# Optimization experiments

Measured on AMD Instinct MI355X. Metric: run time of the kernel, lower is better.

Reference implementation:

```python
import jax, jax.numpy as jnp
import numpy as np

BN_EPS = 1e-5


def _gin_layer(x, src, dst, W1, b1, W2, b2, gamma, beta):
    N = x.shape[0]
    # scatter-add neighbor aggregation (GINConv with eps=0)
    agg = jax.ops.segment_sum(x[src], dst, num_segments=N)
    h = x + agg
    # MLP: Linear -> ReLU -> Linear
    h = jax.nn.relu(h @ W1 + b1) @ W2 + b2
    # BatchNorm1d (training-mode batch statistics, biased variance)
    mean = jnp.mean(h, axis=0)
    var = jnp.mean(jnp.square(h - mean), axis=0)
    h = (h - mean) * jax.lax.rsqrt(var + BN_EPS) * gamma + beta
    return jax.nn.relu(h)


def setup_inputs() -> dict:
    key = jax.random.key(0)
    ks = jax.random.split(key, 16)
    N, E, F_IN, H, L, G, T = 100000, 400000, 128, 256, 5, 4096, 12
    x = jax.random.normal(ks[0], (N, F_IN), dtype=jnp.float32)
    edge_index = jax.random.randint(ks[1], (2, E), 0, N, dtype=jnp.int64)
    batch_idx = jnp.sort(jax.random.randint(ks[2], (N,), 0, G, dtype=jnp.int64))
    s = 0.02
    inp = {
        "x": x,
        "edge_index": edge_index,
        "batch_idx": batch_idx,
        "num_graphs": G,
        # layer 0: 128 -> 256
        "W1_0": jax.random.normal(ks[3], (F_IN, H), dtype=jnp.float32) * s,
        "b1_0": jnp.zeros((H,), jnp.float32),
        "W2_0": jax.random.normal(ks[4], (H, H), dtype=jnp.float32) * s,
        "b2_0": jnp.zeros((H,), jnp.float32),
        "gamma_0": jnp.ones((H,), jnp.float32),
        "beta_0": jnp.zeros((H,), jnp.float32),
        # layers 1..4 stacked: 256 -> 256
        "W1s": jax.random.normal(ks[5], (L - 1, H, H), dtype=jnp.float32) * s,
        "b1s": jnp.zeros((L - 1, H), jnp.float32),
        "W2s": jax.random.normal(ks[6], (L - 1, H, H), dtype=jnp.float32) * s,
        "b2s": jnp.zeros((L - 1, H), jnp.float32),
        "gammas": jnp.ones((L - 1, H), jnp.float32),
        "betas": jnp.zeros((L - 1, H), jnp.float32),
        # predictor
        "Wp1": jax.random.normal(ks[7], (H, H), dtype=jnp.float32) * s,
        "bp1": jnp.zeros((H,), jnp.float32),
        "Wp2": jax.random.normal(ks[8], (H, T), dtype=jnp.float32) * s,
        "bp2": jnp.zeros((T,), jnp.float32),
    }
    return inp


def reference(x, edge_index, batch_idx, num_graphs,
              W1_0, b1_0, W2_0, b2_0, gamma_0, beta_0,
              W1s, b1s, W2s, b2s, gammas, betas,
              Wp1, bp1, Wp2, bp2):
    src, dst = edge_index[0], edge_index[1]
    h = _gin_layer(x, src, dst, W1_0, b1_0, W2_0, b2_0, gamma_0, beta_0)
    for i in range(W1s.shape[0]):
        h = _gin_layer(h, src, dst, W1s[i], b1s[i], W2s[i], b2s[i], gammas[i], betas[i])
    # global mean pool over graphs
    sums = jax.ops.segment_sum(h, batch_idx, num_segments=num_graphs)
    counts = jax.ops.segment_sum(jnp.ones((h.shape[0],), h.dtype), batch_idx, num_segments=num_graphs)
    g = sums / jnp.maximum(counts, 1.0)[:, None]
    # predictor MLP (dropout=0 in eval)
    out = jax.nn.relu(g @ Wp1 + bp1) @ Wp2 + bp2
    return out
```

## Files before the change

### kernel.cpp

```cpp
#include <hip/hip_runtime.h>


typedef __attribute__((ext_vector_type(4))) float f32x4;
typedef __attribute__((ext_vector_type(8))) _Float16 f16x8;

__device__ __forceinline__ float h2f(unsigned short u) {
  _Float16 h; __builtin_memcpy(&h, &u, 2); return (float)h;
}
__device__ __forceinline__ unsigned short f2h16(float f) {
  _Float16 h = (_Float16)f; unsigned short u; __builtin_memcpy(&u, &h, 2); return u;
}
__device__ __forceinline__ unsigned short f2b(float f) {
  union { float f; unsigned int i; } c; c.f = f;
  unsigned int x = c.i;
  return (unsigned short)((x + 0x7fffu + ((x >> 16) & 1u)) >> 16);
}
__device__ __forceinline__ float lin(const void* p, long long i, int wf32) {
  if (wf32) return ((const float*)p)[i];
  union { unsigned int i; float f; } c;
  c.i = ((unsigned int)((const unsigned short*)p)[i]) << 16;
  return c.f;
}
__device__ __forceinline__ int ldidx(const int* p, long long i, int w64) {
  return w64 ? p[2 * i] : p[i];
}

__global__ void detect_k(const int* __restrict__ edge, const unsigned short* __restrict__ xa,
                         int* __restrict__ flags) {
  if (threadIdx.x != 0 || blockIdx.x != 0) return;
  int nzOdd = 0;
  for (int t = 0; t < 256; t++) if (edge[2 * t + 1] != 0) nzOdd++;
  flags[0] = (nzOdd == 0) ? 1 : 0;
  int plaus = 0;
  for (int t = 0; t < 64; t++) {
    unsigned short w = xa[2 * t];
    int e = (w >> 7) & 0xFF;
    if (w == 0 || (e >= 0x70 && e <= 0x85)) plaus++;
  }
  flags[1] = (plaus < 32) ? 1 : 0;
}

__global__ void zero_i32_k(int* __restrict__ p, int n) {
  int i = blockIdx.x * blockDim.x + threadIdx.x;
  if (i < n) p[i] = 0;
}

__global__ void prep_k(const void* __restrict__ b1, const void* __restrict__ b2,
                       const void* __restrict__ gm, const void* __restrict__ bt, int eoff,
                       float* __restrict__ pb1, float* __restrict__ pb2,
                       float* __restrict__ pg, float* __restrict__ pb,
                       float* __restrict__ gsum, const int* __restrict__ flags) {
  int wf32 = flags[1], t = threadIdx.x;
  pb1[t] = lin(b1, (long long)eoff + t, wf32);
  pb2[t] = lin(b2, (long long)eoff + t, wf32);
  pg[t]  = lin(gm, (long long)eoff + t, wf32);
  pb[t]  = lin(bt, (long long)eoff + t, wf32);
  gsum[t] = 0.f; gsum[256 + t] = 0.f;
}
__global__ void copy256_k(const void* __restrict__ src, int eoff, float* __restrict__ dst,
                          const int* __restrict__ flags) {
  dst[threadIdx.x] = lin(src, (long long)eoff + threadIdx.x, flags[1]);
}

__global__ void transpose_off_k(const void* __restrict__ src, long long eoff,
                                unsigned short* __restrict__ dst, int R, int C,
                                const int* __restrict__ flags) {
  int wf32 = flags[1];
  __shared__ unsigned short t[32][33];
  int bx = blockIdx.x * 32, by = blockIdx.y * 32;
  int x = bx + threadIdx.x;
  for (int i = 0; i < 32; i += 8) {
    int y = by + threadIdx.y + i;
    if (y < R && x < C)
      t[threadIdx.y + i][threadIdx.x] = f2h16(lin(src, eoff + (long long)y * C + x, wf32));
  }
  __syncthreads();
  int x2 = by + threadIdx.x;
  for (int i = 0; i < 32; i += 8) {
    int y = bx + threadIdx.y + i;
    if (y < C && x2 < R) dst[(long long)y * R + x2] = t[threadIdx.x][threadIdx.y + i];
  }
}

__global__ void hist_k(const int* __restrict__ edge, int E, int* __restrict__ cnt,
                       const int* __restrict__ flags) {
  int w64 = flags[0];
  int e = blockIdx.x * blockDim.x + threadIdx.x;
  if (e < E) atomicAdd(&cnt[ldidx(edge, (long long)E + e, w64)], 1);
}
#define SCAN_CHUNK 1024
__global__ void scan1_k(const int* __restrict__ in, int* __restrict__ out,
                        int* __restrict__ partials, int n) {
  __shared__ int sh[256];
  int tid = threadIdx.x;
  int base = blockIdx.x * SCAN_CHUNK + tid * 4;
  int v[4]; int tsum = 0;
#pragma unroll
  for (int i = 0; i < 4; i++) { v[i] = (base + i < n) ? in[base + i] : 0; tsum += v[i]; }
  sh[tid] = tsum; __syncthreads();
  for (int off = 1; off < 256; off <<= 1) {
    int t = (tid >= off) ? sh[tid - off] : 0;
    __syncthreads();
    sh[tid] += t;
    __syncthreads();
  }
  int run = sh[tid] - tsum;
#pragma unroll
  for (int i = 0; i < 4; i++) { if (base + i < n) out[base + i] = run; run += v[i]; }
  if (tid == 255) partials[blockIdx.x] = sh[255];
}
__global__ void scan2_k(int* partials, int B) {
  __shared__ int sh[256];
  int tid = threadIdx.x;
  int orig = (tid < B) ? partials[tid] : 0;
  sh[tid] = orig; __syncthreads();
  for (int off = 1; off < 256; off <<= 1) {
    int t = (tid >= off) ? sh[tid - off] : 0;
    __syncthreads();
    sh[tid] += t;
    __syncthreads();
  }
  if (tid < B) partials[tid] = sh[tid] - orig;
}
__global__ void scan3_k(int* __restrict__ out, const int* __restrict__ partials,
                        int n, int total) {
  int base = blockIdx.x * SCAN_CHUNK + threadIdx.x * 4;
  int add = partials[blockIdx.x];
#pragma unroll
  for (int i = 0; i < 4; i++) { if (base + i < n) out[base + i] += add; }
  if (blockIdx.x == 0 && threadIdx.x == 0) out[n] = total;
}
__global__ void fill_k(const int* __restrict__ edge, int E, const int* __restrict__ rowptr,
                       int* __restrict__ cnt, int* __restrict__ colidx,
                       const int* __restrict__ flags) {
  int w64 = flags[0];
  int e = blockIdx.x * blockDim.x + threadIdx.x;
  if (e >= E) return;
  int s = ldidx(edge, e, w64);
  int d = ldidx(edge, (long long)E + e, w64);
  int p = atomicAdd(&cnt[d], 1);
  colidx[rowptr[d] + p] = s;
}
__global__ void graph_bounds_k(const int* __restrict__ b, int Nn, int G,
                               int* __restrict__ gstart, const int* __restrict__ flags) {
  int w64 = flags[0];
  int g = blockIdx.x * blockDim.x + threadIdx.x;
  if (g > G) return;
  int lo = 0, hi = Nn;
  while (lo < hi) {
    int mid = (lo + hi) >> 1;
    if (ldidx(b, mid, w64) < g) lo = mid + 1; else hi = mid;
  }
  gstart[g] = lo;
}

__global__ void convert_k(const void* __restrict__ x, unsigned short* __restrict__ xh,
                          long long n, const int* __restrict__ flags) {
  int wf32 = flags[1];
  long long base = ((long long)blockIdx.x * blockDim.x + threadIdx.x) * 4;
  if (base >= n) return;
#pragma unroll
  for (int k = 0; k < 4; k++) xh[base + k] = f2h16(lin(x, base + k, wf32));
}

template <int LPN, int APPLY>
__global__ void gather_fused_k(const unsigned short* __restrict__ src,
                               const float* __restrict__ scale, const float* __restrict__ shift,
                               const int* __restrict__ rowptr, const int* __restrict__ colidx,
                               unsigned short* __restrict__ u, int Nn) {
  const int F = LPN * 8;
  int gid = blockIdx.x * blockDim.x + threadIdx.x;
  int node = gid / LPN;
  if (node >= Nn) return;
  int fb = (gid % LPN) * 8;
  float sc[8], sh[8];
  if (APPLY) {
#pragma unroll
    for (int k = 0; k < 8; k++) { sc[k] = scale[fb + k]; sh[k] = shift[fb + k]; }
  }
  float acc[8];
  {
    uint4 raw = *(const uint4*)(src + (long long)node * F + fb);
    unsigned int ws[4] = {raw.x, raw.y, raw.z, raw.w};
#pragma unroll
    for (int k = 0; k < 8; k++) {
      float xv = h2f((unsigned short)((ws[k >> 1] >> ((k & 1) * 16)) & 0xffff));
      acc[k] = APPLY ? fmaxf(xv * sc[k] + sh[k], 0.f) : xv;
    }
  }
  int s = rowptr[node], e = rowptr[node + 1];
  for (int j = s; j < e; j++) {
    long long nb = colidx[j];
    uint4 raw = *(const uint4*)(src + nb * F + fb);
    unsigned int ws[4] = {raw.x, raw.y, raw.z, raw.w};
#pragma unroll
    for (int k = 0; k < 8; k++) {
      float xv = h2f((unsigned short)((ws[k >> 1] >> ((k & 1) * 16)) & 0xffff));
      acc[k] += APPLY ? fmaxf(xv * sc[k] + sh[k], 0.f) : xv;
    }
  }
  uint4 o;
  unsigned int wo[4];
#pragma unroll
  for (int p = 0; p < 4; p++)
    wo[p] = (unsigned int)f2h16(acc[2 * p]) | ((unsigned int)f2h16(acc[2 * p + 1]) << 16);
  o.x = wo[0]; o.y = wo[1]; o.z = wo[2]; o.w = wo[3];
  *(uint4*)(u + (long long)node * F + fb) = o;
}

#define SA 40
#define SP 136
__global__ __launch_bounds__(256) void gemm_k(
    const unsigned short* __restrict__ A, const unsigned short* __restrict__ Bt,
    const float* __restrict__ bias, unsigned short* __restrict__ C,
    int M, int K, int relu, float* __restrict__ gsum) {
  __shared__ __align__(16) unsigned short smem[128 * SP];
  unsigned short* As = smem;
  unsigned short* Bs = smem + 128 * SA;
  int m0 = blockIdx.x * 128, n0 = blockIdx.y * 128;
  int tid = threadIdx.x;
  int wave = tid >> 6, lane = tid & 63;
  int wm = (wave >> 1) * 64, wn = (wave & 1) * 64;
  int lrow = lane & 15, lq = lane >> 4;
  f32x4 acc[4][4] = {};
  int ktiles = K >> 5;
  int srow = tid >> 2;
  int ch8 = (tid & 3) << 3;
  int rowA0 = m0 + srow;      rowA0 = rowA0 < M ? rowA0 : M - 1;
  int rowA1 = m0 + srow + 64; rowA1 = rowA1 < M ? rowA1 : M - 1;
  const unsigned short* pa0 = A + (long long)rowA0 * K + ch8;
  const unsigned short* pa1 = A + (long long)rowA1 * K + ch8;
  const unsigned short* pq0 = Bt + (long long)(n0 + srow) * K + ch8;
  const unsigned short* pq1 = Bt + (long long)(n0 + srow + 64) * K + ch8;
  uint4 va0 = *(const uint4*)pa0, va1 = *(const uint4*)pa1;
  uint4 vb0 = *(const uint4*)pq0, vb1 = *(const uint4*)pq1;
  int lo0 = srow * SA + ch8, lo1 = (srow + 64) * SA + ch8;
  for (int kt = 0; kt < ktiles; ++kt) {
    __syncthreads();
    *(uint4*)(As + lo0) = va0;
    *(uint4*)(As + lo1) = va1;
    *(uint4*)(Bs + lo0) = vb0;
    *(uint4*)(Bs + lo1) = vb1;
    __syncthreads();
    f16x8 af[4], bf[4];
#pragma unroll
    for (int r = 0; r < 4; r++)
      af[r] = *(const f16x8*)(As + (wm + 16 * r + lrow) * SA + lq * 8);
#pragma unroll
    for (int c = 0; c < 4; c++)
      bf[c] = *(const f16x8*)(Bs + (wn + 16 * c + lrow) * SA + lq * 8);
    if (kt + 1 < ktiles) {
      int kb = (kt + 1) << 5;
      va0 = *(const uint4*)(pa0 + kb); va1 = *(const uint4*)(pa1 + kb);
      vb0 = *(const uint4*)(pq0 + kb); vb1 = *(const uint4*)(pq1 + kb);
    }
#pragma unroll
    for (int r = 0; r < 4; r++)
#pragma unroll
      for (int c = 0; c < 4; c++)
        acc[r][c] = __builtin_amdgcn_mfma_f32_16x16x32_f16(af[r], bf[c], acc[r][c], 0, 0, 0);
  }
  __syncthreads();
  unsigned short* Ct = smem;
#pragma unroll
  for (int c = 0; c < 4; c++) {
    int col = wn + 16 * c + lrow;
    float bv = bias[n0 + col];
#pragma unroll
    for (int r = 0; r < 4; r++) {
      int rbase = wm + 16 * r + lq * 4;
#pragma unroll
      for (int i = 0; i < 4; i++) {
        float v = acc[r][c][i] + bv;
        if (relu) v = fmaxf(v, 0.f);
        Ct[(rbase + i) * SP + col] = f2h16(v);
      }
    }
  }
  __syncthreads();
  int c16 = tid & 15, g = tid >> 4;
  float s8[8] = {}, q8[8] = {};
  bool dostats = (gsum != nullptr);
#pragma unroll
  for (int i = 0; i < 8; i++) {
    int row = g + i * 16;
    int grow = m0 + row;
    uint4 vw = *(const uint4*)(Ct + row * SP + c16 * 8);
    if (grow < M) {
      *(uint4*)(C + (long long)grow * 256 + n0 + c16 * 8) = vw;
      if (dostats) {
        unsigned int ws[4] = {vw.x, vw.y, vw.z, vw.w};
#pragma unroll
        for (int k = 0; k < 8; k++) {
          float xv = h2f((unsigned short)((ws[k >> 1] >> ((k & 1) * 16)) & 0xffff));
          s8[k] += xv; q8[k] += xv * xv;
        }
      }
    }
  }
  if (dostats) {
    float* shf = (float*)smem;
    __syncthreads();
#pragma unroll
    for (int k = 0; k < 8; k++) shf[(c16 * 8 + k) * 17 + g] = s8[k];
    __syncthreads();
    if (tid < 128) {
      float t = 0.f;
#pragma unroll
      for (int gg = 0; gg < 16; gg++) t += shf[tid * 17 + gg];
      atomicAdd(&gsum[n0 + tid], t);
    }
    __syncthreads();
#pragma unroll
    for (int k = 0; k < 8; k++) shf[(c16 * 8 + k) * 17 + g] = q8[k];
    __syncthreads();
    if (tid < 128) {
      float t = 0.f;
#pragma unroll
      for (int gg = 0; gg < 16; gg++) t += shf[tid * 17 + gg];
      atomicAdd(&gsum[256 + n0 + tid], t);
    }
  }
}

__global__ void bn_finalize_k(const float* __restrict__ gsum,
                              const float* __restrict__ pg, const float* __restrict__ pb,
                              int Nn, float* __restrict__ scale, float* __restrict__ shift) {
  int f = threadIdx.x;
  float inv = 1.f / (float)Nn;
  float mean = gsum[f] * inv;
  float var = fmaxf(gsum[256 + f] * inv - mean * mean, 0.f);
  float sc = pg[f] * rsqrtf(var + 1e-5f);
  scale[f] = sc;
  shift[f] = pb[f] - mean * sc;
}

__global__ void pool_fused_k(const unsigned short* __restrict__ v, const float* __restrict__ scale,
                             const float* __restrict__ shift, const int* __restrict__ gstart,
                             unsigned short* __restrict__ gout) {
  int g = blockIdx.x, f = threadIdx.x;
  int s = gstart[g], e = gstart[g + 1];
  float sc = scale[f], sh = shift[f];
  float acc = 0.f;
  for (int r = s; r < e; r++) acc += fmaxf(h2f(v[(long long)r * 256 + f]) * sc + sh, 0.f);
  gout[(long long)g * 256 + f] = f2h16(acc / fmaxf((float)(e - s), 1.f));
}
__global__ void pred2_k(const unsigned short* __restrict__ p1, const void* __restrict__ Wp2,
                        const void* __restrict__ bp2, void* __restrict__ out, int G,
                        const int* __restrict__ flags) {
  int wf32 = flags[1];
  int idx = blockIdx.x * blockDim.x + threadIdx.x;
  if (idx >= G * 12) return;
  int g = idx / 12, t = idx - g * 12;
  float acc = lin(bp2, t, wf32);
  const unsigned short* row = p1 + (long long)g * 256;
  for (int k = 0; k < 256; k++) acc += h2f(row[k]) * lin(Wp2, k * 12 + t, wf32);
  if (wf32) ((float*)out)[idx] = acc;
  else      ((unsigned short*)out)[idx] = f2b(acc);
}

extern "C" void kernel_launch(void* const* d_in, const int* in_sizes, int n_in,
                              void* d_out, int out_size, void* d_ws, size_t ws_size,
                              hipStream_t stream) {
  int wb = -1;
  for (int i = 3; i + 15 < n_in; i++) {
    if (in_sizes[i] == 32768 && in_sizes[i + 1] == 256 && in_sizes[i + 2] == 65536 &&
        in_sizes[i + 3] == 256 && in_sizes[i + 4] == 256 && in_sizes[i + 5] == 256 &&
        in_sizes[i + 6] == 262144) { wb = i; break; }
  }
  if (wb < 0) wb = (n_in >= 20) ? 4 : 3;

  const void* x      = d_in[0];
  const int*  edge   = (const int*)d_in[1];
  const int*  batch  = (const int*)d_in[2];
  const void* W1_0   = d_in[wb + 0];
  const void* b1_0   = d_in[wb + 1];
  const void* W2_0   = d_in[wb + 2];
  const void* b2_0   = d_in[wb + 3];
  const void* gamma0 = d_in[wb + 4];
  const void* beta0  = d_in[wb + 5];
  const void* W1s    = d_in[wb + 6];
  const void* b1s    = d_in[wb + 7];
  const void* W2s    = d_in[wb + 8];
  const void* b2s    = d_in[wb + 9];
  const void* gammas = d_in[wb + 10];
  const void* betas  = d_in[wb + 11];
  const void* Wp1    = d_in[wb + 12];
  const void* bp1    = d_in[wb + 13];
  const void* Wp2    = d_in[wb + 14];
  const void* bp2    = d_in[wb + 15];

  const int N = in_sizes[0] / 128;
  const int E = in_sizes[1] / 2;
  const int G = out_size / 12;
  const int H = 256;

  char* w = (char*)d_ws;
  size_t off = 0;
  auto alloc = [&](size_t bytes) -> char* {
    char* p = w + off;
    off += (bytes + 255) & ~(size_t)255;
    return p;
  };
  unsigned short* bufX  = (unsigned short*)alloc((size_t)N * H * 2);
  unsigned short* bufY  = (unsigned short*)alloc((size_t)N * H * 2);
  unsigned short* w1_0t = (unsigned short*)alloc((size_t)128 * 256 * 2);
  unsigned short* w2_0t = (unsigned short*)alloc((size_t)256 * 256 * 2);
  unsigned short* w1st  = (unsigned short*)alloc((size_t)4 * 256 * 256 * 2);
  unsigned short* w2st  = (unsigned short*)alloc((size_t)4 * 256 * 256 * 2);
  unsigned short* wp1t  = (unsigned short*)alloc((size_t)256 * 256 * 2);
  int*   rowptr   = (int*)alloc((size_t)(N + 1) * 4);
  int*   cnt      = (int*)alloc((size_t)N * 4);
  int*   colidx   = (int*)alloc((size_t)E * 4);
  int*   partials = (int*)alloc(1024 * 4);
  float* gsum     = (float*)alloc(512 * 4);
  float* bnscale  = (float*)alloc(256 * 4);
  float* bnshift  = (float*)alloc(256 * 4);
  float* pg       = (float*)alloc(256 * 4);
  float* pb       = (float*)alloc(256 * 4);
  float* pb1      = (float*)alloc(256 * 4);
  float* pb2      = (float*)alloc(256 * 4);
  int*   gstart   = (int*)alloc((size_t)(G + 1) * 4);
  int*   flags    = (int*)alloc(256);
  unsigned short* gpool = (unsigned short*)alloc((size_t)G * H * 2);
  unsigned short* p1    = (unsigned short*)alloc((size_t)G * H * 2);
  (void)ws_size; (void)n_in;

  detect_k<<<1, 64, 0, stream>>>(edge, (const unsigned short*)x, flags);

  convert_k<<<(int)(((long long)N * 128 / 4 + 255) / 256), 256, 0, stream>>>(
      x, bufY, (long long)N * 128, flags);

  dim3 tb(32, 8);
  auto transpose = [&](const void* src, long long eoff, unsigned short* dst, int R, int C) {
    transpose_off_k<<<dim3((C + 31) / 32, (R + 31) / 32), tb, 0, stream>>>(src, eoff, dst, R, C, flags);
  };
  transpose(W1_0, 0, w1_0t, 128, 256);
  transpose(W2_0, 0, w2_0t, 256, 256);
  for (int i = 0; i < 4; i++) {
    transpose(W1s, (long long)i * 65536, w1st + i * 65536, 256, 256);
    transpose(W2s, (long long)i * 65536, w2st + i * 65536, 256, 256);
  }
  transpose(Wp1, 0, wp1t, 256, 256);

  zero_i32_k<<<(N + 255) / 256, 256, 0, stream>>>(cnt, N);
  hist_k<<<(E + 255) / 256, 256, 0, stream>>>(edge, E, cnt, flags);
  int NB = (N + SCAN_CHUNK - 1) / SCAN_CHUNK;
  scan1_k<<<NB, 256, 0, stream>>>(cnt, rowptr, partials, N);
  scan2_k<<<1, 256, 0, stream>>>(partials, NB);
  scan3_k<<<NB, 256, 0, stream>>>(rowptr, partials, N, E);
  zero_i32_k<<<(N + 255) / 256, 256, 0, stream>>>(cnt, N);
  fill_k<<<(E + 255) / 256, 256, 0, stream>>>(edge, E, rowptr, cnt, colidx, flags);
  graph_bounds_k<<<(G + 1 + 255) / 256, 256, 0, stream>>>(batch, N, G, gstart, flags);

  auto gemm = [&](const unsigned short* A, const unsigned short* Bt, const float* bias,
                  unsigned short* Cq, int M, int K, int relu, float* stats) {
    gemm_k<<<dim3((M + 127) / 128, 2), 256, 0, stream>>>(A, Bt, bias, Cq, M, K, relu, stats);
  };

  prep_k<<<1, 256, 0, stream>>>(b1_0, b2_0, gamma0, beta0, 0, pb1, pb2, pg, pb, gsum, flags);
  gather_fused_k<16, 0><<<(N * 16 + 255) / 256, 256, 0, stream>>>(
      bufY, bnscale, bnshift, rowptr, colidx, bufX, N);
  gemm(bufX, w1_0t, pb1, bufY, N, 128, 1, nullptr);
  gemm(bufY, w2_0t, pb2, bufX, N, 256, 0, gsum);
  bn_finalize_k<<<1, 256, 0, stream>>>(gsum, pg, pb, N, bnscale, bnshift);
  unsigned short* cur = bufX;
  unsigned short* oth = bufY;
  for (int i = 0; i < 4; i++) {
    prep_k<<<1, 256, 0, stream>>>(b1s, b2s, gammas, betas, i * 256, pb1, pb2, pg, pb, gsum, flags);
    gather_fused_k<32, 1><<<(N * 32 + 255) / 256, 256, 0, stream>>>(
        cur, bnscale, bnshift, rowptr, colidx, oth, N);
    gemm(oth, w1st + i * 65536, pb1, cur, N, 256, 1, nullptr);
    gemm(cur, w2st + i * 65536, pb2, oth, N, 256, 0, gsum);
    bn_finalize_k<<<1, 256, 0, stream>>>(gsum, pg, pb, N, bnscale, bnshift);
    unsigned short* t = cur; cur = oth; oth = t;
  }

  copy256_k<<<1, 256, 0, stream>>>(bp1, 0, pb1, flags);
  pool_fused_k<<<G, 256, 0, stream>>>(cur, bnscale, bnshift, gstart, gpool);
  gemm(gpool, wp1t, pb1, p1, G, 256, 1, nullptr);
  pred2_k<<<(G * 12 + 255) / 256, 256, 0, stream>>>(p1, Wp2, bp2, d_out, G, flags);
}
```

Before: 981.7 us.

## Fuse both MLP GEMMs per GIN layer into a persistent kernel

Replaces the two separate GEMM launches per layer with one persistent kernel that keeps each 128-row tile's hidden activation in LDS, computes Linear->ReLU->Linear, writes the output and accumulates BatchNorm statistics. It also prefetches the next tile into a second LDS buffer and uses XOR-swizzled LDS layouts. The goal is to remove the global write and re-read of the 256-wide intermediate and to cut launch count. In exchange it uses 128 KB of LDS with 512 threads, which limits occupancy, reads the weights straight from global memory inside the MFMA loop, and fixes the grid at 256 blocks.

New measurement: 1.326 ms. 35.1% more time.

```diff
diff --git a/kernel.cpp b/kernel.cpp
--- a/kernel.cpp
+++ b/kernel.cpp
@@ -208,6 +208,169 @@
   *(uint4*)(u + (long long)node * F + fb) = o;
 }
 
+template <int KIN>
+__global__ __launch_bounds__(512, 2) void fused_layer_k(
+    const unsigned short* __restrict__ A, const unsigned short* __restrict__ W1t,
+    const unsigned short* __restrict__ W2t, const float* __restrict__ b1,
+    const float* __restrict__ b2, unsigned short* __restrict__ V,
+    int M, int ntiles, float* __restrict__ gsum) {
+  __shared__ __align__(16) unsigned char lds_raw[131072];
+  const int tid = threadIdx.x;
+  const int lane = tid & 63, wave = tid >> 6;
+  const int l15 = lane & 15, lq = lane >> 4;
+  const int wn = wave >> 1, wm = wave & 1;
+  const int nb0 = wn * 64, mb0 = wm * 64;
+  constexpr int KT1 = KIN / 32;
+  const int srow = tid >> 2;
+  const int sc0 = tid & 3;
+
+  if ((int)blockIdx.x < ntiles) {
+    long long m0 = (long long)blockIdx.x * 128;
+    long long row = m0 + srow; if (row >= M) row = M - 1;
+    const unsigned short* ps = A + row * KIN + sc0 * 8;
+#pragma unroll
+    for (int j = 0; j < KT1; j++) {
+      int c = sc0 + 4 * j;
+      uint4 v = *(const uint4*)(ps + 32 * j);
+      *(uint4*)(lds_raw + srow * (2 * KIN) + 16 * (c ^ (srow & 7))) = v;
+    }
+  }
+  __syncthreads();
+
+  unsigned char* Rp = lds_raw;
+  unsigned char* Rq = lds_raw + 65536;
+  for (int t = blockIdx.x; t < ntiles; t += 256) {
+    long long m0 = (long long)t * 128;
+    int tn = t + 256;
+    bool hasNext = tn < ntiles;
+    uint4 pre[KT1];
+    if (hasNext) {
+      long long rowN = (long long)tn * 128 + srow;
+      if (rowN >= M) rowN = M - 1;
+      const unsigned short* ps = A + rowN * KIN + sc0 * 8;
+#pragma unroll
+      for (int j = 0; j < KT1; j++) pre[j] = *(const uint4*)(ps + 32 * j);
+    }
+    f32x4 acc[4][4] = {};
+#pragma unroll
+    for (int kt = 0; kt < KT1; kt++) {
+      f16x8 wf[4], uf[4];
+#pragma unroll
+      for (int r = 0; r < 4; r++)
+        wf[r] = *(const f16x8*)(W1t + (long long)(nb0 + 16 * r + l15) * KIN + kt * 32 + lq * 8);
+#pragma unroll
+      for (int c = 0; c < 4; c++) {
+        int m = mb0 + 16 * c + l15;
+        uf[c] = *(const f16x8*)(Rp + m * (2 * KIN) + 16 * ((kt * 4 + lq) ^ (m & 7)));
+      }
+#pragma unroll
+      for (int r = 0; r < 4; r++)
+#pragma unroll
+        for (int c = 0; c < 4; c++)
+          acc[r][c] = __builtin_amdgcn_mfma_f32_16x16x32_f16(wf[r], uf[c], acc[r][c], 0, 0, 0);
+    }
+    __syncthreads();
+#pragma unroll
+    for (int r = 0; r < 4; r++) {
+      int nbase = nb0 + 16 * r + lq * 4;
+      float4 bv = *(const float4*)(b1 + nbase);
+#pragma unroll
+      for (int c = 0; c < 4; c++) {
+        int m = mb0 + 16 * c + l15;
+        unsigned int h0 = f2h16(fmaxf(acc[r][c][0] + bv.x, 0.f));
+        unsigned int h1v = f2h16(fmaxf(acc[r][c][1] + bv.y, 0.f));
+        unsigned int h2v = f2h16(fmaxf(acc[r][c][2] + bv.z, 0.f));
+        unsigned int h3 = f2h16(fmaxf(acc[r][c][3] + bv.w, 0.f));
+        uint2 pk; pk.x = h0 | (h1v << 16); pk.y = h2v | (h3 << 16);
+        int by = m * 512 + 16 * ((nbase >> 3) ^ (m & 7)) + ((nbase & 7) << 1);
+        *(uint2*)(Rp + by) = pk;
+      }
+    }
+    if (hasNext) {
+#pragma unroll
+      for (int j = 0; j < KT1; j++) {
+        int c = sc0 + 4 * j;
+        *(uint4*)(Rq + srow * (2 * KIN) + 16 * (c ^ (srow & 7))) = pre[j];
+      }
+    }
+    __syncthreads();
+    f32x4 acc2[4][4] = {};
+#pragma unroll
+    for (int kt = 0; kt < 8; kt++) {
+      f16x8 wf[4], hf[4];
+#pragma unroll
+      for (int r = 0; r < 4; r++)
+        wf[r] = *(const f16x8*)(W2t + (long long)(nb0 + 16 * r + l15) * 256 + kt * 32 + lq * 8);
+#pragma unroll
+      for (int c = 0; c < 4; c++) {
+        int m = mb0 + 16 * c + l15;
+        hf[c] = *(const f16x8*)(Rp + m * 512 + 16 * ((kt * 4 + lq) ^ (m & 7)));
+      }
+#pragma unroll
+      for (int r = 0; r < 4; r++)
+#pragma unroll
+        for (int c = 0; c < 4; c++)
+          acc2[r][c] = __builtin_amdgcn_mfma_f32_16x16x32_f16(wf[r], hf[c], acc2[r][c], 0, 0, 0);
+    }
+    __syncthreads();
+#pragma unroll
+    for (int r = 0; r < 4; r++) {
+      int nbase = nb0 + 16 * r + lq * 4;
+      float4 bv = *(const float4*)(b2 + nbase);
+#pragma unroll
+      for (int c = 0; c < 4; c++) {
+        int m = mb0 + 16 * c + l15;
+        unsigned int h0 = f2h16(acc2[r][c][0] + bv.x);
+        unsigned int h1v = f2h16(acc2[r][c][1] + bv.y);
+        unsigned int h2v = f2h16(acc2[r][c][2] + bv.z);
+        unsigned int h3 = f2h16(acc2[r][c][3] + bv.w);
+        uint2 pk; pk.x = h0 | (h1v << 16); pk.y = h2v | (h3 << 16);
+        int by = m * 512 + 16 * ((nbase >> 3) ^ (m & 7)) + ((nbase & 7) << 1);
+        *(uint2*)(Rp + by) = pk;
+      }
+    }
+    __syncthreads();
+    const int c32 = tid & 31, rg = tid >> 5;
+    float s8[8] = {}, q8[8] = {};
+#pragma unroll
+    for (int k = 0; k < 8; k++) {
+      int m = rg * 8 + k;
+      uint4 vw = *(const uint4*)(Rp + m * 512 + 16 * (c32 ^ (m & 7)));
+      long long grow = m0 + m;
+      if (grow < M) {
+        *(uint4*)(V + grow * 256 + c32 * 8) = vw;
+        unsigned int ws[4] = {vw.x, vw.y, vw.z, vw.w};
+#pragma unroll
+        for (int kk = 0; kk < 8; kk++) {
+          float xv = h2f((unsigned short)((ws[kk >> 1] >> ((kk & 1) * 16)) & 0xffff));
+          s8[kk] += xv; q8[kk] += xv * xv;
+        }
+      }
+    }
+    __syncthreads();
+    float* shf = (float*)Rp;
+#pragma unroll
+    for (int kk = 0; kk < 8; kk++) {
+      int col = c32 * 8 + kk;
+      shf[col * 17 + rg] = s8[kk];
+      shf[4352 + col * 17 + rg] = q8[kk];
+    }
+    __syncthreads();
+    if (tid < 256) {
+      float tot = 0.f;
+#pragma unroll
+      for (int g = 0; g < 16; g++) tot += shf[tid * 17 + g];
+      atomicAdd(&gsum[tid], tot);
+    } else {
+      int col = tid - 256; float tot = 0.f;
+#pragma unroll
+      for (int g = 0; g < 16; g++) tot += shf[4352 + col * 17 + g];
+      atomicAdd(&gsum[256 + col], tot);
+    }
+    unsigned char* tmp = Rp; Rp = Rq; Rq = tmp;
+  }
+}
+
 #define SA 40
 #define SP 136
 __global__ __launch_bounds__(256) void gemm_k(
@@ -220,8 +383,8 @@
   int m0 = blockIdx.x * 128, n0 = blockIdx.y * 128;
   int tid = threadIdx.x;
   int wave = tid >> 6, lane = tid & 63;
-  int wm = (wave >> 1) * 64, wn = (wave & 1) * 64;
-  int lrow = lane & 15, lq = lane >> 4;
+  int wm = (wave >> 1) * 64, wnn = (wave & 1) * 64;
+  int lrow = lane & 15, lqq = lane >> 4;
   f32x4 acc[4][4] = {};
   int ktiles = K >> 5;
   int srow = tid >> 2;
@@ -245,10 +408,10 @@
     f16x8 af[4], bf[4];
 #pragma unroll
     for (int r = 0; r < 4; r++)
-      af[r] = *(const f16x8*)(As + (wm + 16 * r + lrow) * SA + lq * 8);
+      af[r] = *(const f16x8*)(As + (wm + 16 * r + lrow) * SA + lqq * 8);
 #pragma unroll
     for (int c = 0; c < 4; c++)
-      bf[c] = *(const f16x8*)(Bs + (wn + 16 * c + lrow) * SA + lq * 8);
+      bf[c] = *(const f16x8*)(Bs + (wnn + 16 * c + lrow) * SA + lqq * 8);
     if (kt + 1 < ktiles) {
       int kb = (kt + 1) << 5;
       va0 = *(const uint4*)(pa0 + kb); va1 = *(const uint4*)(pa1 + kb);
@@ -264,11 +427,11 @@
   unsigned short* Ct = smem;
 #pragma unroll
   for (int c = 0; c < 4; c++) {
-    int col = wn + 16 * c + lrow;
+    int col = wnn + 16 * c + lrow;
     float bv = bias[n0 + col];
 #pragma unroll
     for (int r = 0; r < 4; r++) {
-      int rbase = wm + 16 * r + lq * 4;
+      int rbase = wm + 16 * r + lqq * 4;
 #pragma unroll
       for (int i = 0; i < 4; i++) {
         float v = acc[r][c][i] + bv;
@@ -453,31 +616,32 @@
   fill_k<<<(E + 255) / 256, 256, 0, stream>>>(edge, E, rowptr, cnt, colidx, flags);
   graph_bounds_k<<<(G + 1 + 255) / 256, 256, 0, stream>>>(batch, N, G, gstart, flags);
 
-  auto gemm = [&](const unsigned short* A, const unsigned short* Bt, const float* bias,
-                  unsigned short* Cq, int M, int K, int relu, float* stats) {
-    gemm_k<<<dim3((M + 127) / 128, 2), 256, 0, stream>>>(A, Bt, bias, Cq, M, K, relu, stats);
+  const int ntiles = (N + 127) / 128;
+  auto fused = [&](const unsigned short* Au, const unsigned short* w1, const unsigned short* w2,
+                   unsigned short* Vv, int K) {
+    if (K == 128)
+      fused_layer_k<128><<<256, 512, 0, stream>>>(Au, w1, w2, pb1, pb2, Vv, N, ntiles, gsum);
+    else
+      fused_layer_k<256><<<256, 512, 0, stream>>>(Au, w1, w2, pb1, pb2, Vv, N, ntiles, gsum);
   };
 
   prep_k<<<1, 256, 0, stream>>>(b1_0, b2_0, gamma0, beta0, 0, pb1, pb2, pg, pb, gsum, flags);
   gather_fused_k<16, 0><<<(N * 16 + 255) / 256, 256, 0, stream>>>(
       bufY, bnscale, bnshift, rowptr, colidx, bufX, N);
-  gemm(bufX, w1_0t, pb1, bufY, N, 128, 1, nullptr);
-  gemm(bufY, w2_0t, pb2, bufX, N, 256, 0, gsum);
+  fused(bufX, w1_0t, w2_0t, bufY, 128);
   bn_finalize_k<<<1, 256, 0, stream>>>(gsum, pg, pb, N, bnscale, bnshift);
-  unsigned short* cur = bufX;
-  unsigned short* oth = bufY;
+  unsigned short* cur = bufY;
+  unsigned short* oth = bufX;
   for (int i = 0; i < 4; i++) {
     prep_k<<<1, 256, 0, stream>>>(b1s, b2s, gammas, betas, i * 256, pb1, pb2, pg, pb, gsum, flags);
     gather_fused_k<32, 1><<<(N * 32 + 255) / 256, 256, 0, stream>>>(
         cur, bnscale, bnshift, rowptr, colidx, oth, N);
-    gemm(oth, w1st + i * 65536, pb1, cur, N, 256, 1, nullptr);
-    gemm(cur, w2st + i * 65536, pb2, oth, N, 256, 0, gsum);
+    fused(oth, w1st + i * 65536, w2st + i * 65536, cur, 256);
     bn_finalize_k<<<1, 256, 0, stream>>>(gsum, pg, pb, N, bnscale, bnshift);
-    unsigned short* t = cur; cur = oth; oth = t;
   }
 
   copy256_k<<<1, 256, 0, stream>>>(bp1, 0, pb1, flags);
   pool_fused_k<<<G, 256, 0, stream>>>(cur, bnscale, bnshift, gstart, gpool);
-  gemm(gpool, wp1t, pb1, p1, G, 256, 1, nullptr);
+  gemm_k<<<dim3((G + 127) / 128, 2), 256, 0, stream>>>(gpool, wp1t, pb1, p1, G, 256, 1, nullptr);
   pred2_k<<<(G * 12 + 255) / 256, 256, 0, stream>>>(p1, Wp2, bp2, d_out, G, flags);
 }
```
